# Performance work log

Measured on AMD Instinct MI355X. Metric: run time of the kernel, lower is better.

## Reference

```python
import jax, jax.numpy as jnp
import numpy as np

N_LEVELS = 16
BASE_RES = 16.0
MAX_RES = 128.0
LOG2_T = 19
T_SIZE = 2 ** LOG2_T
F = 2

# primes wrapped to int32 to mimic torch int32 overflow semantics
P0 = np.int32(1)
P1 = np.int32(np.uint32(2654435761))
P2 = np.int32(np.uint32(805459861))

# corner offsets matching (c_000,c_100,c_010,c_001,c_110,c_101,c_011,c_111)
OFFSETS = np.array([[0,0,0],[1,0,0],[0,1,0],[0,0,1],
                    [1,1,0],[1,0,1],[0,1,1],[1,1,1]], dtype=np.int32)


def setup_inputs() -> dict:
    key = jax.random.key(0)
    k1, k2 = jax.random.split(key)
    x = jax.random.uniform(k1, (1048576, 3), dtype=jnp.float32)
    hashtable = jax.random.uniform(k2, (T_SIZE, F), dtype=jnp.float32) * 2.0 - 1.0
    return {"x": x, "hashtable": hashtable}


def _resolutions():
    growth = np.exp((np.log(MAX_RES) - np.log(BASE_RES)) / (N_LEVELS - 1))
    return np.floor(BASE_RES * growth ** np.arange(N_LEVELS)).astype(np.float32)  # [L]


def reference(x, hashtable):
    res = jnp.asarray(_resolutions())                      # [L]
    xs = x[None, :, :] * res[:, None, None]                # [L,N,3]
    xf = jnp.floor(xs)
    xfi = xf.astype(jnp.int32)                             # [L,N,3]
    xci = jnp.ceil(xs).astype(jnp.int32)                   # [L,N,3]
    d = xs - xf                                            # [L,N,3] interp weights

    off = jnp.asarray(OFFSETS)[:, None, None, :]           # [8,1,1,3]
    corners = jnp.where(off == 1, xci[None], xfi[None])    # [8,L,N,3]

    h = (corners[..., 0] * P0) ^ (corners[..., 1] * P1) ^ (corners[..., 2] * P2)
    h = jnp.mod(h, T_SIZE)                                 # [8,L,N], nonnegative

    v = hashtable[h]                                       # [8,L,N,F]

    w = jnp.where(off == 1, d[None], 1.0 - d[None])        # [8,L,N,3]
    w = jnp.prod(w, axis=-1)                               # [8,L,N]

    enc = jnp.sum(v * w[..., None], axis=0)                # [L,N,F]
    N = x.shape[0]
    return jnp.transpose(enc, (1, 0, 2)).reshape(N, N_LEVELS * F)
```

## Files before the change

### kernel.cpp

```cpp
#include <hip/hip_runtime.h>


__constant__ float c_res[16] = {
    16.f, 18.f, 21.f, 24.f, 27.f, 32.f, 36.f, 42.f,
    48.f, 55.f, 64.f, 73.f, 84.f, 97.f, 111.f, 128.f
};

#define TMASK   0x7FFFFu
#define PRIME1  2654435761u
#define PRIME2  805459861u
#define NBUCKET 4096
#define NB      256
#define NGRP    16
#define CACHE_N 4467

__device__ __forceinline__ int bucket_of(float x0, float x1, float x2) {
    int c0 = (int)(x0 * 16.f); c0 = c0 < 0 ? 0 : (c0 > 15 ? 15 : c0);
    int c1 = (int)(x1 * 16.f); c1 = c1 < 0 ? 0 : (c1 > 15 ? 15 : c1);
    int c2 = (int)(x2 * 16.f); c2 = c2 < 0 ? 0 : (c2 > 15 ? 15 : c2);
    return (c0 << 8) | (c1 << 4) | c2;
}

__global__ __launch_bounds__(1024)
void k_histA(const float* __restrict__ x, unsigned* __restrict__ cnt,
             unsigned* __restrict__ grpsum, int npts)
{
    __shared__ unsigned h[NBUCKET];
    for (int j = threadIdx.x; j < NBUCKET; j += 1024) h[j] = 0u;
    __syncthreads();
    int chunk = (npts + NB - 1) / NB;
    int begin = blockIdx.x * chunk;
    int end   = begin + chunk; if (end > npts) end = npts;
    for (int i = begin + threadIdx.x; i < end; i += 1024) {
        int b = bucket_of(x[3 * i], x[3 * i + 1], x[3 * i + 2]);
        atomicAdd(&h[b], 1u);
    }
    __syncthreads();
    unsigned* grow = grpsum + (size_t)(blockIdx.x >> 4) * NBUCKET;
    for (int j = threadIdx.x; j < NBUCKET; j += 1024) {
        unsigned v = h[j];
        cnt[(size_t)blockIdx.x * NBUCKET + j] = v;
        if (v) atomicAdd(&grow[j], v);
    }
}

__global__ __launch_bounds__(1024)
void k_scatB(const float* __restrict__ x, const unsigned* __restrict__ cnt,
             const unsigned* __restrict__ grpsum, unsigned* __restrict__ starts,
             unsigned* __restrict__ perm, int npts)
{
    __shared__ unsigned cur[NBUCKET];
    __shared__ unsigned tmp[1024];
    const int t   = threadIdx.x;
    const int blk = blockIdx.x;
    const int myg = blk >> 4;
    const int r0  = blk & ~15;

    const uint4* gs4 = (const uint4*)grpsum;
    const uint4* ct4 = (const uint4*)cnt;
    uint4 tot = make_uint4(0u,0u,0u,0u), bas = make_uint4(0u,0u,0u,0u);
    #pragma unroll
    for (int g = 0; g < NGRP; ++g) {
        uint4 v = gs4[g * 1024 + t];
        tot.x += v.x; tot.y += v.y; tot.z += v.z; tot.w += v.w;
        if (g < myg) { bas.x += v.x; bas.y += v.y; bas.z += v.z; bas.w += v.w; }
    }
    for (int r = r0; r < blk; ++r) {
        uint4 v = ct4[r * 1024 + t];
        bas.x += v.x; bas.y += v.y; bas.z += v.z; bas.w += v.w;
    }
    unsigned s = tot.x + tot.y + tot.z + tot.w;
    tmp[t] = s;
    __syncthreads();
    for (int off = 1; off < 1024; off <<= 1) {
        unsigned u = (t >= off) ? tmp[t - off] : 0u;
        __syncthreads();
        tmp[t] += u;
        __syncthreads();
    }
    unsigned excl = tmp[t] - s;
    unsigned s0 = excl, s1 = s0 + tot.x, s2 = s1 + tot.y, s3 = s2 + tot.z;
    cur[4*t+0] = s0 + bas.x;
    cur[4*t+1] = s1 + bas.y;
    cur[4*t+2] = s2 + bas.z;
    cur[4*t+3] = s3 + bas.w;
    if (blk == 0) {
        starts[4*t+0] = s0; starts[4*t+1] = s1;
        starts[4*t+2] = s2; starts[4*t+3] = s3;
        if (t == 1023) starts[NBUCKET] = tmp[1023];
    }
    __syncthreads();

    int chunk = (npts + NB - 1) / NB;
    int begin = blk * chunk;
    int end   = begin + chunk; if (end > npts) end = npts;
    for (int i = begin + t; i < end; i += 1024) {
        float x0 = x[3 * i], x1 = x[3 * i + 1], x2 = x[3 * i + 2];
        int b = bucket_of(x0, x1, x2);
        unsigned pos = atomicAdd(&cur[b], 1u);
        perm[pos] = (unsigned)i;
    }
}

__global__ __launch_bounds__(256)
void k_gather(const float* __restrict__ x, const unsigned* __restrict__ perm,
              float4* __restrict__ xs, int npts)
{
    int i = blockIdx.x * 256 + threadIdx.x;
    if (i >= npts) return;
    unsigned p = perm[i];
    float4 v;
    v.x = x[3 * p]; v.y = x[3 * p + 1]; v.z = x[3 * p + 2];
    v.w = __uint_as_float(p);
    xs[i] = v;
}


template<int MODE>
__global__ __launch_bounds__(512, 8)
void k_main(const float4* __restrict__ xs, const float* __restrict__ x,
            const unsigned* __restrict__ perm,
            const unsigned* __restrict__ starts, const float2* __restrict__ tab,
            float4* __restrict__ out4)
{
    __shared__ float2 cache[CACHE_N];
    __shared__ int4 metaA[16];
    __shared__ int4 metaB[16];

    int cell = blockIdx.x;
    int startp = starts[cell], endp = starts[cell + 1];
    if (startp == endp) return;

    int ci = (cell >> 8) & 15, cj = (cell >> 4) & 15, ck = cell & 15;
    float fi0 = ci * 0.0625f, fi1 = (ci + 1) * 0.0625f;
    float fj0 = cj * 0.0625f, fj1 = (cj + 1) * 0.0625f;
    float fk0 = ck * 0.0625f, fk1 = (ck + 1) * 0.0625f;

    int cbase = 0;
    #pragma unroll 1
    for (int l = 0; l < 16; ++l) {
        float r = c_res[l];
        int lo0 = (int)floorf(fi0 * r), hi0 = (int)ceilf(fi1 * r);
        int lo1 = (int)floorf(fj0 * r), hi1 = (int)ceilf(fj1 * r);
        int lo2 = (int)floorf(fk0 * r), hi2 = (int)ceilf(fk1 * r);
        int n0 = hi0 - lo0 + 1, n1 = hi1 - lo1 + 1, n2 = hi2 - lo2 + 1;
        int n12 = n1 * n2, tot = n0 * n12;
        for (int t = threadIdx.x; t < tot; t += 512) {
            int a = t / n12, rem = t - a * n12;
            int b = rem / n2, d = rem - b * n2;
            unsigned h = ((unsigned)(lo0 + a)
                        ^ ((unsigned)(lo1 + b) * PRIME1)
                        ^ ((unsigned)(lo2 + d) * PRIME2)) & TMASK;
            cache[cbase + t] = tab[h];
        }
        if (threadIdx.x == 0) {
            metaA[l] = make_int4(lo0, lo1, lo2, cbase);
            metaB[l] = make_int4(n12, n2, __float_as_int(r), 0);
        }
        cbase += tot;
    }
    __syncthreads();

    auto lvl = [&](int l, float a0, float a1, float a2, float& ex, float& ey) {
        int4 mA = metaA[l];
        int4 mB = metaB[l];
        float r = __int_as_float(mB.z);
        int n12 = mB.x, n2 = mB.y;
        float s0 = a0 * r, s1 = a1 * r, s2 = a2 * r;
        float f0 = floorf(s0), f1 = floorf(s1), f2 = floorf(s2);
        float d0 = s0 - f0, d1 = s1 - f1, d2 = s2 - f2;
        int A0 = (int)f0 - mA.x, A1 = (int)f1 - mA.y, A2 = (int)f2 - mA.z;
        int e0 = (d0 != 0.f) ? n12 : 0;
        int e1 = (d1 != 0.f) ? n2  : 0;
        int e2 = (d2 != 0.f) ? 1   : 0;
        int rA = mA.w + A0 * n12 + A1 * n2 + A2;

        float2 v0 = cache[rA];
        float2 v1 = cache[rA + e0];
        float2 v2 = cache[rA + e1];
        float2 v3 = cache[rA + e2];
        float2 v4 = cache[rA + e0 + e1];
        float2 v5 = cache[rA + e0 + e2];
        float2 v6 = cache[rA + e1 + e2];
        float2 v7 = cache[rA + e0 + e1 + e2];

        float u0 = 1.f - d0, u1 = 1.f - d1, u2 = 1.f - d2;
        float pa = u1 * u2, pb = d1 * u2, pc = u1 * d2, pe = d1 * d2;
        float w0 = u0 * pa, w1 = d0 * pa, w2 = u0 * pb, w3 = u0 * pc;
        float w4 = d0 * pb, w5 = d0 * pc, w6 = u0 * pe, w7 = d0 * pe;

        float rx = v0.x * w0, ry = v0.y * w0;
        rx += v1.x * w1;  ry += v1.y * w1;
        rx += v2.x * w2;  ry += v2.y * w2;
        rx += v3.x * w3;  ry += v3.y * w3;
        rx += v4.x * w4;  ry += v4.y * w4;
        rx += v5.x * w5;  ry += v5.y * w5;
        rx += v6.x * w6;  ry += v6.y * w6;
        rx += v7.x * w7;  ry += v7.y * w7;
        ex = rx; ey = ry;
    };

    for (int sp = startp + (int)threadIdx.x; sp < endp; sp += 512) {
        float x0, x1, x2; unsigned p;
        if constexpr (MODE == 0) {
            float4 v = xs[sp];
            x0 = v.x; x1 = v.y; x2 = v.z; p = __float_as_uint(v.w);
        } else {
            p = perm[sp];
            x0 = x[3 * p]; x1 = x[3 * p + 1]; x2 = x[3 * p + 2];
        }
        #pragma unroll 1
        for (int lp = 0; lp < 8; ++lp) {
            float4 o;
            lvl(2 * lp,     x0, x1, x2, o.x, o.y);
            lvl(2 * lp + 1, x0, x1, x2, o.z, o.w);
            out4[(size_t)p * 8 + lp] = o;
        }
    }
}

__global__ __launch_bounds__(256, 8)
void k_fallback(const float* __restrict__ x, const float2* __restrict__ tab,
                float2* __restrict__ out, int total) {
    int tid = blockIdx.x * 256 + threadIdx.x;
    if (tid >= total) return;
    int p = tid >> 4, l = tid & 15;
    float r = c_res[l];
    float s0 = x[3*p] * r, s1 = x[3*p+1] * r, s2 = x[3*p+2] * r;
    float f0 = floorf(s0), f1 = floorf(s1), f2 = floorf(s2);
    float d0 = s0 - f0, d1 = s1 - f1, d2 = s2 - f2;
    unsigned A0 = (unsigned)(int)f0, B0 = (unsigned)(int)ceilf(s0);
    unsigned A1 = (unsigned)(int)f1 * PRIME1, B1 = (unsigned)(int)ceilf(s1) * PRIME1;
    unsigned A2 = (unsigned)(int)f2 * PRIME2, B2 = (unsigned)(int)ceilf(s2) * PRIME2;
    unsigned h0=(A0^A1^A2)&TMASK, h1=(B0^A1^A2)&TMASK, h2=(A0^B1^A2)&TMASK;
    unsigned h3=(A0^A1^B2)&TMASK, h4=(B0^B1^A2)&TMASK, h5=(B0^A1^B2)&TMASK;
    unsigned h6=(A0^B1^B2)&TMASK, h7=(B0^B1^B2)&TMASK;
    float2 v0=tab[h0],v1=tab[h1],v2=tab[h2],v3=tab[h3];
    float2 v4=tab[h4],v5=tab[h5],v6=tab[h6],v7=tab[h7];
    float u0=1.f-d0,u1=1.f-d1,u2=1.f-d2;
    float ex = v0.x*(u0*u1*u2), ey = v0.y*(u0*u1*u2);
    ex += v1.x*(d0*u1*u2); ey += v1.y*(d0*u1*u2);
    ex += v2.x*(u0*d1*u2); ey += v2.y*(u0*d1*u2);
    ex += v3.x*(u0*u1*d2); ey += v3.y*(u0*u1*d2);
    ex += v4.x*(d0*d1*u2); ey += v4.y*(d0*d1*u2);
    ex += v5.x*(d0*u1*d2); ey += v5.y*(d0*u1*d2);
    ex += v6.x*(u0*d1*d2); ey += v6.y*(u0*d1*d2);
    ex += v7.x*(d0*d1*d2); ey += v7.y*(d0*d1*d2);
    float2 o; o.x = ex; o.y = ey; out[tid] = o;
}

extern "C" void kernel_launch(void* const* d_in, const int* in_sizes, int n_in,
                              void* d_out, int out_size, void* d_ws, size_t ws_size,
                              hipStream_t stream)
{
    const float*  x   = (const float*)d_in[0];
    const float2* tab = (const float2*)d_in[1];
    int npts = in_sizes[0] / 3;

    size_t off_grpsum = 0;
    size_t off_cnt    = off_grpsum + (size_t)NGRP * NBUCKET * 4;
    size_t off_starts = off_cnt    + (size_t)NB * NBUCKET * 4;
    size_t off_perm   = (off_starts + (size_t)(NBUCKET + 1) * 4 + 63)
                        & ~(size_t)63;
    size_t off_xs     = (off_perm + (size_t)npts * 4 + 63) & ~(size_t)63;

    {
        size_t need = off_xs + (size_t)npts * 16;
        if (ws_size >= need) {
            unsigned* grpsum = (unsigned*)((char*)d_ws + off_grpsum);
            unsigned* cnt    = (unsigned*)((char*)d_ws + off_cnt);
            unsigned* starts = (unsigned*)((char*)d_ws + off_starts);
            unsigned* perm   = (unsigned*)((char*)d_ws + off_perm);
            float4*   xs     = (float4*)  ((char*)d_ws + off_xs);

            hipMemsetAsync(grpsum, 0, (size_t)NGRP * NBUCKET * 4, stream);
            k_histA   <<<NB, 1024, 0, stream>>>(x, cnt, grpsum, npts);
            k_scatB   <<<NB, 1024, 0, stream>>>(x, cnt, grpsum, starts,
                                                perm, npts);
            k_gather  <<<(npts + 255) / 256, 256, 0, stream>>>(x, perm,
                                                               xs, npts);
            k_main<0> <<<NBUCKET, 512, 0, stream>>>(xs, x, nullptr, starts,
                                                    tab, (float4*)d_out);
            return;
        }
    }

    {
        size_t need = off_perm + (size_t)npts * 4;
        if (ws_size >= need) {
            unsigned* grpsum = (unsigned*)((char*)d_ws + off_grpsum);
            unsigned* cnt    = (unsigned*)((char*)d_ws + off_cnt);
            unsigned* starts = (unsigned*)((char*)d_ws + off_starts);
            unsigned* perm   = (unsigned*)((char*)d_ws + off_perm);

            hipMemsetAsync(grpsum, 0, (size_t)NGRP * NBUCKET * 4, stream);
            k_histA   <<<NB, 1024, 0, stream>>>(x, cnt, grpsum, npts);
            k_scatB   <<<NB, 1024, 0, stream>>>(x, cnt, grpsum, starts,
                                                perm, npts);
            k_main<1> <<<NBUCKET, 512, 0, stream>>>(nullptr, x, perm, starts,
                                                    tab, (float4*)d_out);
            return;
        }
    }

    int total = npts * 16;
    k_fallback<<<(total + 255) / 256, 256, 0, stream>>>(
        x, tab, (float2*)d_out, total);
}
```

Baseline: 263.6 us.

## Replace histogram-scan-scatter-gather with fixed-capacity bucket scatter plus overflow path

The sort pipeline (histogram, prefix-scan scatter, gather) is replaced by a single kernel that counts per-block buckets, reserves slots with global atomics, and writes packed float4 points directly into fixed-capacity per-cell slots. Points that exceed the capacity go to an overflow list, which the main kernel handles with a direct hashtable-lookup path after its cell work. This removes two kernel launches and the intermediate perm array traffic. In exchange it uses a sparser padded buffer, adds global atomics, and loses global contiguity of the point stream.

```diff
diff --git a/kernel.cpp b/kernel.cpp
--- a/kernel.cpp
+++ b/kernel.cpp
@@ -19,6 +19,43 @@
     int c1 = (int)(x1 * 16.f); c1 = c1 < 0 ? 0 : (c1 > 15 ? 15 : c1);
     int c2 = (int)(x2 * 16.f); c2 = c2 < 0 ? 0 : (c2 > 15 ? 15 : c2);
     return (c0 << 8) | (c1 << 4) | c2;
+}
+
+__global__ __launch_bounds__(1024)
+void k_scat1(const float* __restrict__ x, unsigned* __restrict__ cnt,
+             unsigned* __restrict__ ovfcnt, unsigned* __restrict__ ovfl,
+             float4* __restrict__ xs, int npts, int cap, int ovfl_cap)
+{
+    __shared__ unsigned h[NBUCKET];
+    for (int j = threadIdx.x; j < NBUCKET; j += 1024) h[j] = 0u;
+    __syncthreads();
+    int chunk = (npts + NB - 1) / NB;
+    int begin = blockIdx.x * chunk;
+    int end   = begin + chunk; if (end > npts) end = npts;
+
+    for (int i = begin + threadIdx.x; i < end; i += 1024) {
+        int b = bucket_of(x[3*i], x[3*i+1], x[3*i+2]);
+        atomicAdd(&h[b], 1u);
+    }
+    __syncthreads();
+    for (int j = threadIdx.x; j < NBUCKET; j += 1024) {
+        unsigned v = h[j];
+        if (v) h[j] = atomicAdd(&cnt[j], v);
+    }
+    __syncthreads();
+    for (int i = begin + threadIdx.x; i < end; i += 1024) {
+        float x0 = x[3*i], x1 = x[3*i+1], x2 = x[3*i+2];
+        int b = bucket_of(x0, x1, x2);
+        unsigned slot = atomicAdd(&h[b], 1u);
+        if (slot < (unsigned)cap) {
+            float4 v; v.x = x0; v.y = x1; v.z = x2;
+            v.w = __uint_as_float((unsigned)i);
+            xs[(size_t)b * cap + slot] = v;
+        } else {
+            unsigned o = atomicAdd(ovfcnt, 1u);
+            if (o < (unsigned)ovfl_cap) ovfl[o] = (unsigned)i;
+        }
+    }
 }
 
 __global__ __launch_bounds__(1024)
@@ -102,17 +139,44 @@
     }
 }
 
-__global__ __launch_bounds__(256)
-void k_gather(const float* __restrict__ x, const unsigned* __restrict__ perm,
-              float4* __restrict__ xs, int npts)
-{
-    int i = blockIdx.x * 256 + threadIdx.x;
-    if (i >= npts) return;
-    unsigned p = perm[i];
-    float4 v;
-    v.x = x[3 * p]; v.y = x[3 * p + 1]; v.z = x[3 * p + 2];
-    v.w = __uint_as_float(p);
-    xs[i] = v;
+__device__ __forceinline__ void point_direct(const float* __restrict__ x,
+                                             const float2* __restrict__ tab,
+                                             float4* __restrict__ out4,
+                                             unsigned p)
+{
+    float a0 = x[3*p], a1 = x[3*p+1], a2 = x[3*p+2];
+    #pragma unroll 1
+    for (int lp = 0; lp < 8; ++lp) {
+        float4 o;
+        #pragma unroll
+        for (int half = 0; half < 2; ++half) {
+            int l = 2 * lp + half;
+            float r = c_res[l];
+            float s0 = a0 * r, s1 = a1 * r, s2 = a2 * r;
+            float f0 = floorf(s0), f1 = floorf(s1), f2 = floorf(s2);
+            float d0 = s0 - f0, d1 = s1 - f1, d2 = s2 - f2;
+            unsigned A0 = (unsigned)(int)f0, B0 = (unsigned)(int)ceilf(s0);
+            unsigned A1 = (unsigned)(int)f1 * PRIME1,
+                     B1 = (unsigned)(int)ceilf(s1) * PRIME1;
+            unsigned A2 = (unsigned)(int)f2 * PRIME2,
+                     B2 = (unsigned)(int)ceilf(s2) * PRIME2;
+            float2 v0 = tab[(A0^A1^A2)&TMASK], v1 = tab[(B0^A1^A2)&TMASK];
+            float2 v2 = tab[(A0^B1^A2)&TMASK], v3 = tab[(A0^A1^B2)&TMASK];
+            float2 v4 = tab[(B0^B1^A2)&TMASK], v5 = tab[(B0^A1^B2)&TMASK];
+            float2 v6 = tab[(A0^B1^B2)&TMASK], v7 = tab[(B0^B1^B2)&TMASK];
+            float u0 = 1.f-d0, u1 = 1.f-d1, u2 = 1.f-d2;
+            float ex = v0.x*(u0*u1*u2), ey = v0.y*(u0*u1*u2);
+            ex += v1.x*(d0*u1*u2); ey += v1.y*(d0*u1*u2);
+            ex += v2.x*(u0*d1*u2); ey += v2.y*(u0*d1*u2);
+            ex += v3.x*(u0*u1*d2); ey += v3.y*(u0*u1*d2);
+            ex += v4.x*(d0*d1*u2); ey += v4.y*(d0*d1*u2);
+            ex += v5.x*(d0*u1*d2); ey += v5.y*(d0*u1*d2);
+            ex += v6.x*(u0*d1*d2); ey += v6.y*(u0*d1*d2);
+            ex += v7.x*(d0*d1*d2); ey += v7.y*(d0*d1*d2);
+            if (half) { o.z = ex; o.w = ey; } else { o.x = ex; o.y = ey; }
+        }
+        out4[(size_t)p * 8 + lp] = o;
+    }
 }
 
 
@@ -121,101 +185,121 @@
 void k_main(const float4* __restrict__ xs, const float* __restrict__ x,
             const unsigned* __restrict__ perm,
             const unsigned* __restrict__ starts, const float2* __restrict__ tab,
-            float4* __restrict__ out4)
+            float4* __restrict__ out4, const unsigned* __restrict__ cnt,
+            const unsigned* __restrict__ ovfcnt,
+            const unsigned* __restrict__ ovfl, int cap, int ovfl_cap)
 {
     __shared__ float2 cache[CACHE_N];
     __shared__ int4 metaA[16];
     __shared__ int4 metaB[16];
 
     int cell = blockIdx.x;
-    int startp = starts[cell], endp = starts[cell + 1];
-    if (startp == endp) return;
-
-    int ci = (cell >> 8) & 15, cj = (cell >> 4) & 15, ck = cell & 15;
-    float fi0 = ci * 0.0625f, fi1 = (ci + 1) * 0.0625f;
-    float fj0 = cj * 0.0625f, fj1 = (cj + 1) * 0.0625f;
-    float fk0 = ck * 0.0625f, fk1 = (ck + 1) * 0.0625f;
-
-    int cbase = 0;
-    #pragma unroll 1
-    for (int l = 0; l < 16; ++l) {
-        float r = c_res[l];
-        int lo0 = (int)floorf(fi0 * r), hi0 = (int)ceilf(fi1 * r);
-        int lo1 = (int)floorf(fj0 * r), hi1 = (int)ceilf(fj1 * r);
-        int lo2 = (int)floorf(fk0 * r), hi2 = (int)ceilf(fk1 * r);
-        int n0 = hi0 - lo0 + 1, n1 = hi1 - lo1 + 1, n2 = hi2 - lo2 + 1;
-        int n12 = n1 * n2, tot = n0 * n12;
-        for (int t = threadIdx.x; t < tot; t += 512) {
-            int a = t / n12, rem = t - a * n12;
-            int b = rem / n2, d = rem - b * n2;
-            unsigned h = ((unsigned)(lo0 + a)
-                        ^ ((unsigned)(lo1 + b) * PRIME1)
-                        ^ ((unsigned)(lo2 + d) * PRIME2)) & TMASK;
-            cache[cbase + t] = tab[h];
-        }
-        if (threadIdx.x == 0) {
-            metaA[l] = make_int4(lo0, lo1, lo2, cbase);
-            metaB[l] = make_int4(n12, n2, __float_as_int(r), 0);
-        }
-        cbase += tot;
-    }
-    __syncthreads();
-
-    auto lvl = [&](int l, float a0, float a1, float a2, float& ex, float& ey) {
-        int4 mA = metaA[l];
-        int4 mB = metaB[l];
-        float r = __int_as_float(mB.z);
-        int n12 = mB.x, n2 = mB.y;
-        float s0 = a0 * r, s1 = a1 * r, s2 = a2 * r;
-        float f0 = floorf(s0), f1 = floorf(s1), f2 = floorf(s2);
-        float d0 = s0 - f0, d1 = s1 - f1, d2 = s2 - f2;
-        int A0 = (int)f0 - mA.x, A1 = (int)f1 - mA.y, A2 = (int)f2 - mA.z;
-        int e0 = (d0 != 0.f) ? n12 : 0;
-        int e1 = (d1 != 0.f) ? n2  : 0;
-        int e2 = (d2 != 0.f) ? 1   : 0;
-        int rA = mA.w + A0 * n12 + A1 * n2 + A2;
-
-        float2 v0 = cache[rA];
-        float2 v1 = cache[rA + e0];
-        float2 v2 = cache[rA + e1];
-        float2 v3 = cache[rA + e2];
-        float2 v4 = cache[rA + e0 + e1];
-        float2 v5 = cache[rA + e0 + e2];
-        float2 v6 = cache[rA + e1 + e2];
-        float2 v7 = cache[rA + e0 + e1 + e2];
-
-        float u0 = 1.f - d0, u1 = 1.f - d1, u2 = 1.f - d2;
-        float pa = u1 * u2, pb = d1 * u2, pc = u1 * d2, pe = d1 * d2;
-        float w0 = u0 * pa, w1 = d0 * pa, w2 = u0 * pb, w3 = u0 * pc;
-        float w4 = d0 * pb, w5 = d0 * pc, w6 = u0 * pe, w7 = d0 * pe;
-
-        float rx = v0.x * w0, ry = v0.y * w0;
-        rx += v1.x * w1;  ry += v1.y * w1;
-        rx += v2.x * w2;  ry += v2.y * w2;
-        rx += v3.x * w3;  ry += v3.y * w3;
-        rx += v4.x * w4;  ry += v4.y * w4;
-        rx += v5.x * w5;  ry += v5.y * w5;
-        rx += v6.x * w6;  ry += v6.y * w6;
-        rx += v7.x * w7;  ry += v7.y * w7;
-        ex = rx; ey = ry;
-    };
-
-    for (int sp = startp + (int)threadIdx.x; sp < endp; sp += 512) {
-        float x0, x1, x2; unsigned p;
-        if constexpr (MODE == 0) {
-            float4 v = xs[sp];
-            x0 = v.x; x1 = v.y; x2 = v.z; p = __float_as_uint(v.w);
-        } else {
-            p = perm[sp];
-            x0 = x[3 * p]; x1 = x[3 * p + 1]; x2 = x[3 * p + 2];
-        }
+    int startp, endp;
+    if constexpr (MODE == 0) {
+        unsigned cn = cnt[cell];
+        if (cn > (unsigned)cap) cn = (unsigned)cap;
+        startp = cell * cap;
+        endp   = startp + (int)cn;
+    } else {
+        startp = starts[cell]; endp = starts[cell + 1];
+    }
+
+    if (startp < endp) {
+        int ci = (cell >> 8) & 15, cj = (cell >> 4) & 15, ck = cell & 15;
+        float fi0 = ci * 0.0625f, fi1 = (ci + 1) * 0.0625f;
+        float fj0 = cj * 0.0625f, fj1 = (cj + 1) * 0.0625f;
+        float fk0 = ck * 0.0625f, fk1 = (ck + 1) * 0.0625f;
+
+        int cbase = 0;
         #pragma unroll 1
-        for (int lp = 0; lp < 8; ++lp) {
-            float4 o;
-            lvl(2 * lp,     x0, x1, x2, o.x, o.y);
-            lvl(2 * lp + 1, x0, x1, x2, o.z, o.w);
-            out4[(size_t)p * 8 + lp] = o;
-        }
+        for (int l = 0; l < 16; ++l) {
+            float r = c_res[l];
+            int lo0 = (int)floorf(fi0 * r), hi0 = (int)ceilf(fi1 * r);
+            int lo1 = (int)floorf(fj0 * r), hi1 = (int)ceilf(fj1 * r);
+            int lo2 = (int)floorf(fk0 * r), hi2 = (int)ceilf(fk1 * r);
+            int n0 = hi0 - lo0 + 1, n1 = hi1 - lo1 + 1, n2 = hi2 - lo2 + 1;
+            int n12 = n1 * n2, tot = n0 * n12;
+            for (int t = threadIdx.x; t < tot; t += 512) {
+                int a = t / n12, rem = t - a * n12;
+                int b = rem / n2, d = rem - b * n2;
+                unsigned hh = ((unsigned)(lo0 + a)
+                            ^ ((unsigned)(lo1 + b) * PRIME1)
+                            ^ ((unsigned)(lo2 + d) * PRIME2)) & TMASK;
+                cache[cbase + t] = tab[hh];
+            }
+            if (threadIdx.x == 0) {
+                metaA[l] = make_int4(lo0, lo1, lo2, cbase);
+                metaB[l] = make_int4(n12, n2, __float_as_int(r), 0);
+            }
+            cbase += tot;
+        }
+        __syncthreads();
+
+        auto lvl = [&](int l, float a0, float a1, float a2,
+                       float& ex, float& ey) {
+            int4 mA = metaA[l];
+            int4 mB = metaB[l];
+            float r = __int_as_float(mB.z);
+            int n12 = mB.x, n2 = mB.y;
+            float s0 = a0 * r, s1 = a1 * r, s2 = a2 * r;
+            float f0 = floorf(s0), f1 = floorf(s1), f2 = floorf(s2);
+            float d0 = s0 - f0, d1 = s1 - f1, d2 = s2 - f2;
+            int A0 = (int)f0 - mA.x, A1 = (int)f1 - mA.y, A2 = (int)f2 - mA.z;
+            int e0 = (d0 != 0.f) ? n12 : 0;
+            int e1 = (d1 != 0.f) ? n2  : 0;
+            int e2 = (d2 != 0.f) ? 1   : 0;
+            int rA = mA.w + A0 * n12 + A1 * n2 + A2;
+
+            float2 v0 = cache[rA];
+            float2 v1 = cache[rA + e0];
+            float2 v2 = cache[rA + e1];
+            float2 v3 = cache[rA + e2];
+            float2 v4 = cache[rA + e0 + e1];
+            float2 v5 = cache[rA + e0 + e2];
+            float2 v6 = cache[rA + e1 + e2];
+            float2 v7 = cache[rA + e0 + e1 + e2];
+
+            float u0 = 1.f - d0, u1 = 1.f - d1, u2 = 1.f - d2;
+            float pa = u1 * u2, pb = d1 * u2, pc = u1 * d2, pe = d1 * d2;
+            float w0 = u0 * pa, w1 = d0 * pa, w2 = u0 * pb, w3 = u0 * pc;
+            float w4 = d0 * pb, w5 = d0 * pc, w6 = u0 * pe, w7 = d0 * pe;
+
+            float rx = v0.x * w0, ry = v0.y * w0;
+            rx += v1.x * w1;  ry += v1.y * w1;
+            rx += v2.x * w2;  ry += v2.y * w2;
+            rx += v3.x * w3;  ry += v3.y * w3;
+            rx += v4.x * w4;  ry += v4.y * w4;
+            rx += v5.x * w5;  ry += v5.y * w5;
+            rx += v6.x * w6;  ry += v6.y * w6;
+            rx += v7.x * w7;  ry += v7.y * w7;
+            ex = rx; ey = ry;
+        };
+
+        for (int sp = startp + (int)threadIdx.x; sp < endp; sp += 512) {
+            float x0, x1, x2; unsigned p;
+            if constexpr (MODE == 0) {
+                float4 v = xs[sp];
+                x0 = v.x; x1 = v.y; x2 = v.z; p = __float_as_uint(v.w);
+            } else {
+                p = perm[sp];
+                x0 = x[3 * p]; x1 = x[3 * p + 1]; x2 = x[3 * p + 2];
+            }
+            #pragma unroll 1
+            for (int lp = 0; lp < 8; ++lp) {
+                float4 o;
+                lvl(2 * lp,     x0, x1, x2, o.x, o.y);
+                lvl(2 * lp + 1, x0, x1, x2, o.z, o.w);
+                out4[(size_t)p * 8 + lp] = o;
+            }
+        }
+    }
+
+    if constexpr (MODE == 0) {
+        unsigned ovfn = *ovfcnt;
+        if (ovfn > (unsigned)ovfl_cap) ovfn = (unsigned)ovfl_cap;
+        for (unsigned u = blockIdx.x * 512u + threadIdx.x; u < ovfn;
+             u += 4096u * 512u)
+            point_direct(x, tab, out4, ovfl[u]);
     }
 }
 
@@ -257,48 +341,56 @@
     const float2* tab = (const float2*)d_in[1];
     int npts = in_sizes[0] / 3;
 
-    size_t off_grpsum = 0;
-    size_t off_cnt    = off_grpsum + (size_t)NGRP * NBUCKET * 4;
-    size_t off_starts = off_cnt    + (size_t)NB * NBUCKET * 4;
-    size_t off_perm   = (off_starts + (size_t)(NBUCKET + 1) * 4 + 63)
-                        & ~(size_t)63;
-    size_t off_xs     = (off_perm + (size_t)npts * 4 + 63) & ~(size_t)63;
-
     {
-        size_t need = off_xs + (size_t)npts * 16;
+        size_t off_cnt  = 0;
+        size_t off_ovfc = off_cnt + (size_t)NBUCKET * 4;
+        size_t off_ovfl = (off_ovfc + 64 + 63) & ~(size_t)63;
+        size_t off_xs   = (off_ovfl + (size_t)npts * 4 + 255) & ~(size_t)255;
+        if (ws_size > off_xs) {
+            size_t avail = ws_size - off_xs;
+            long long capll = (long long)(avail / ((size_t)NBUCKET * 16));
+            int cap = (int)(capll > 512 ? 512 : capll);
+            int mean = npts / NBUCKET + 1;
+            if (cap >= mean + (mean + 3) / 4 + 64) {
+                unsigned* cnt    = (unsigned*)((char*)d_ws + off_cnt);
+                unsigned* ovfc   = (unsigned*)((char*)d_ws + off_ovfc);
+                unsigned* ovfl   = (unsigned*)((char*)d_ws + off_ovfl);
+                float4*   xs     = (float4*)  ((char*)d_ws + off_xs);
+
+                hipMemsetAsync((char*)d_ws + off_cnt, 0,
+                               (size_t)NBUCKET * 4 + 64, stream);
+                k_scat1 <<<NB, 1024, 0, stream>>>(x, cnt, ovfc, ovfl, xs,
+                                                  npts, cap, npts);
+                k_main<0><<<NBUCKET, 512, 0, stream>>>(xs, x, nullptr, nullptr,
+                                                       tab, (float4*)d_out,
+                                                       cnt, ovfc, ovfl,
+                                                       cap, npts);
+                return;
+            }
+        }
+    }
+
+    {
+        size_t off_grpsum = 0;
+        size_t off_cnt    = off_grpsum + (size_t)NGRP * NBUCKET * 4;
+        size_t off_starts = off_cnt    + (size_t)NB * NBUCKET * 4;
+        size_t off_perm   = (off_starts + (size_t)(NBUCKET + 1) * 4 + 63)
+                            & ~(size_t)63;
+        size_t need       = off_perm + (size_t)npts * 4;
         if (ws_size >= need) {
             unsigned* grpsum = (unsigned*)((char*)d_ws + off_grpsum);
             unsigned* cnt    = (unsigned*)((char*)d_ws + off_cnt);
             unsigned* starts = (unsigned*)((char*)d_ws + off_starts);
             unsigned* perm   = (unsigned*)((char*)d_ws + off_perm);
-            float4*   xs     = (float4*)  ((char*)d_ws + off_xs);
-
-            hipMemsetAsync(grpsum, 0, (size_t)NGRP * NBUCKET * 4, stream);
-            k_histA   <<<NB, 1024, 0, stream>>>(x, cnt, grpsum, npts);
-            k_scatB   <<<NB, 1024, 0, stream>>>(x, cnt, grpsum, starts,
-                                                perm, npts);
-            k_gather  <<<(npts + 255) / 256, 256, 0, stream>>>(x, perm,
-                                                               xs, npts);
-            k_main<0> <<<NBUCKET, 512, 0, stream>>>(xs, x, nullptr, starts,
-                                                    tab, (float4*)d_out);
-            return;
-        }
-    }
-
-    {
-        size_t need = off_perm + (size_t)npts * 4;
-        if (ws_size >= need) {
-            unsigned* grpsum = (unsigned*)((char*)d_ws + off_grpsum);
-            unsigned* cnt    = (unsigned*)((char*)d_ws + off_cnt);
-            unsigned* starts = (unsigned*)((char*)d_ws + off_starts);
-            unsigned* perm   = (unsigned*)((char*)d_ws + off_perm);
 
             hipMemsetAsync(grpsum, 0, (size_t)NGRP * NBUCKET * 4, stream);
             k_histA   <<<NB, 1024, 0, stream>>>(x, cnt, grpsum, npts);
             k_scatB   <<<NB, 1024, 0, stream>>>(x, cnt, grpsum, starts,
                                                 perm, npts);
             k_main<1> <<<NBUCKET, 512, 0, stream>>>(nullptr, x, perm, starts,
-                                                    tab, (float4*)d_out);
+                                                    tab, (float4*)d_out,
+                                                    nullptr, nullptr, nullptr,
+                                                    0, 0);
             return;
         }
     }
```

After: 242.1 us. -8.1%, faster.
